# Performance work log

Hardware: AMD Instinct MI355X
Metric: run time of the kernel (lower is better)

The kernel has to match this reference:

```python
import jax, jax.numpy as jnp
import numpy as np

N_NODES = 156
NFEAT = 256
NHID = 128
B = 16384
T = 24
HLSTM = 32
ALPHA = 0.2


def setup_inputs() -> dict:
    key = jax.random.key(0)
    ks = jax.random.split(key, 16)
    f32 = jnp.float32
    inp = {
        "embedding": jax.random.normal(ks[0], (N_NODES, NFEAT), f32),
        "x": jax.random.normal(ks[1], (B, T, N_NODES), f32),
        "adj": jax.random.randint(ks[2], (N_NODES, N_NODES), 0, 2, jnp.int32),
        # GAT params (xavier-ish scale)
        "W_recent": jax.random.normal(ks[3], (NFEAT, NHID), f32) * 0.08,
        "a_recent": jax.random.normal(ks[4], (2 * NHID, 1), f32) * 0.1,
        "W_period": jax.random.normal(ks[5], (NFEAT, NHID), f32) * 0.08,
        "a_period": jax.random.normal(ks[6], (2 * NHID, 1), f32) * 0.1,
        # LSTM params, torch layout: weight_ih [4H, D], weight_hh [4H, H]
        "Wih_r": jax.random.normal(ks[7], (4 * HLSTM, N_NODES), f32) * 0.08,
        "Whh_r": jax.random.normal(ks[8], (4 * HLSTM, HLSTM), f32) * 0.08,
        "bih_r": jnp.zeros((4 * HLSTM,), f32),
        "bhh_r": jnp.zeros((4 * HLSTM,), f32),
        "Wih_p": jax.random.normal(ks[9], (4 * HLSTM, N_NODES), f32) * 0.08,
        "Whh_p": jax.random.normal(ks[10], (4 * HLSTM, HLSTM), f32) * 0.08,
        "bih_p": jnp.zeros((4 * HLSTM,), f32),
        "bhh_p": jnp.zeros((4 * HLSTM,), f32),
        "fc_W": jax.random.normal(ks[11], (N_NODES, 2 * HLSTM), f32) * 0.1,
        "fc_b": jnp.zeros((N_NODES,), f32),
    }
    return inp


def _gat_attention(embedding, W, a, adj):
    # h = embedding @ W : [N, F]
    h = embedding @ W
    F = h.shape[1]
    # e[i,j] = leakyrelu(h_i . a[:F] + h_j . a[F:])  (same math as the
    # repeat/cat construction, without materializing [N*N, 2F])
    s1 = h @ a[:F, 0]   # [N]
    s2 = h @ a[F:, 0]   # [N]
    e = jax.nn.leaky_relu(s1[:, None] + s2[None, :], ALPHA)
    e = jnp.where(adj > 0, e, jnp.float32(-9e15))
    return jax.nn.softmax(e, axis=1)  # [N, N]


def _lstm_last(x_seq, Wih, Whh, bih, bhh):
    # x_seq: [B, T, D]; returns last hidden state [B, H]
    H = Whh.shape[1]
    Bn = x_seq.shape[0]
    h0 = jnp.zeros((Bn, H), x_seq.dtype)
    c0 = jnp.zeros((Bn, H), x_seq.dtype)
    bias = bih + bhh

    def step(carry, xt):
        h, c = carry
        g = xt @ Wih.T + h @ Whh.T + bias
        i, f, gg, o = jnp.split(g, 4, axis=-1)  # torch gate order i,f,g,o
        c = jax.nn.sigmoid(f) * c + jax.nn.sigmoid(i) * jnp.tanh(gg)
        h = jax.nn.sigmoid(o) * jnp.tanh(c)
        return (h, c), None

    (h, c), _ = jax.lax.scan(step, (h0, c0), jnp.swapaxes(x_seq, 0, 1))
    return h


def reference(embedding, x, adj, W_recent, a_recent, W_period, a_period,
              Wih_r, Whh_r, bih_r, bhh_r, Wih_p, Whh_p, bih_p, bhh_p,
              fc_W, fc_b):
    recent = x[:, :4, :]   # [B, 4, N]
    period = x[:, 4:, :]   # [B, T-4, N]

    # attention depends only on embedding/adj -> identical across timesteps
    attn_r = _gat_attention(embedding, W_recent, a_recent, adj)  # [N, N]
    attn_p = _gat_attention(embedding, W_period, a_period, adj)

    # out[b,t,i] = sum_j attn[i,j] * x[b,t,j]
    xr = jnp.einsum('ij,btj->bti', attn_r, recent)
    xp = jnp.einsum('ij,btj->bti', attn_p, period)

    hr = _lstm_last(xr, Wih_r, Whh_r, bih_r, bhh_r)  # [B, 32]
    hp = _lstm_last(xp, Wih_p, Whh_p, bih_p, bhh_p)  # [B, 32]

    h = jnp.concatenate([hr, hp], axis=1)            # [B, 64]
    return h @ fc_W.T + fc_b                         # [B, 156]
```

## Files before the change

### kernel.cpp

```cpp
#include <hip/hip_runtime.h>
#include <hip/hip_bf16.h>
#include <math.h>

#define N_NODES 156
#define NFEAT 256
#define NHID 128
#define BATCH 16384
#define TT 24
#define HLSTM 32
#define G4 128
#define ALPHA 0.2f
#define NW 2
#define ROWS_B (NW*16)

typedef __attribute__((ext_vector_type(8))) short bf16x8;
typedef __attribute__((ext_vector_type(4))) float f32x4;

static __device__ __forceinline__ unsigned short f2bf(float f) {
    unsigned u = __float_as_uint(f);
    u += 0x7fffu + ((u >> 16) & 1u);
    return (unsigned short)(u >> 16);
}
static __device__ __forceinline__ bf16x8 cv8(float4 a, float4 b) {
    union { __hip_bfloat16 h[8]; bf16x8 v; } u;
    u.h[0] = __float2bfloat16(a.x); u.h[1] = __float2bfloat16(a.y);
    u.h[2] = __float2bfloat16(a.z); u.h[3] = __float2bfloat16(a.w);
    u.h[4] = __float2bfloat16(b.x); u.h[5] = __float2bfloat16(b.y);
    u.h[6] = __float2bfloat16(b.z); u.h[7] = __float2bfloat16(b.w);
    return u.v;
}
static __device__ __forceinline__ float sigm(float x) { return 1.f / (1.f + __expf(-x)); }
static __device__ __forceinline__ float tanh_(float x) { return 1.f - 2.f / (__expf(2.f * x) + 1.f); }

__global__ void k_gat_s(const float* __restrict__ emb,
                        const float* __restrict__ Wr, const float* __restrict__ ar,
                        const float* __restrict__ Wp, const float* __restrict__ ap,
                        float* __restrict__ s_buf ) {
    int i = blockIdx.x;
    int gat = blockIdx.y;
    const float* W = gat ? Wp : Wr;
    const float* a = gat ? ap : ar;
    int j = threadIdx.x;
    __shared__ float erow[NFEAT];
    __shared__ float red[128];
    for (int k = j; k < NFEAT; k += 128) erow[k] = emb[i*NFEAT + k];
    __syncthreads();
    float h = 0.f;
    for (int k = 0; k < NFEAT; ++k) h = fmaf(erow[k], W[k*NHID + j], h);
    float v1 = h * a[j];
    float v2 = h * a[NHID + j];
    red[j] = v1; __syncthreads();
    for (int s = 64; s > 0; s >>= 1) { if (j < s) red[j] += red[j+s]; __syncthreads(); }
    if (j == 0) s_buf[(gat*2+0)*N_NODES + i] = red[0];
    __syncthreads();
    red[j] = v2; __syncthreads();
    for (int s = 64; s > 0; s >>= 1) { if (j < s) red[j] += red[j+s]; __syncthreads(); }
    if (j == 0) s_buf[(gat*2+1)*N_NODES + i] = red[0];
}

__global__ void k_attn(const float* __restrict__ s_buf, const int* __restrict__ adj,
                       float* __restrict__ attn ) {
    int i = blockIdx.x, gat = blockIdx.y;
    int j = threadIdx.x;
    __shared__ float red[256];
    float s1 = s_buf[(gat*2+0)*N_NODES + i];
    bool act = (j < N_NODES);
    float e = -INFINITY;
    if (act) {
        float s2 = s_buf[(gat*2+1)*N_NODES + j];
        float z = s1 + s2;
        z = (z > 0.f) ? z : ALPHA * z;
        if (adj[i*N_NODES + j] <= 0) z = -9e15f;
        e = z;
    }
    red[j] = e; __syncthreads();
    for (int s = 128; s > 0; s >>= 1) { if (j < s) red[j] = fmaxf(red[j], red[j+s]); __syncthreads(); }
    float m = red[0]; __syncthreads();
    float val = act ? __expf(e - m) : 0.f;
    red[j] = val; __syncthreads();
    for (int s = 128; s > 0; s >>= 1) { if (j < s) red[j] += red[j+s]; __syncthreads(); }
    float inv = 1.f / red[0];
    if (act) attn[(gat*N_NODES + i)*N_NODES + j] = val * inv;
}

__global__ void k_prep(const float* __restrict__ attn,
                       const float* __restrict__ Wih_r, const float* __restrict__ Wih_p,
                       const float* __restrict__ Whh_r, const float* __restrict__ Whh_p,
                       const float* __restrict__ bih_r, const float* __restrict__ bhh_r,
                       const float* __restrict__ bih_p, const float* __restrict__ bhh_p,
                       unsigned short* __restrict__ Mbf ,
                       unsigned short* __restrict__ Whhbf ,
                       float* __restrict__ bias2 ) {
    int g = blockIdx.x, gat = blockIdx.y;
    const float* Wih = gat ? Wih_p : Wih_r;
    const float* A = attn + gat*N_NODES*N_NODES;
    int j = threadIdx.x;
    if (j < 160) {
        float acc = 0.f;
        if (j < N_NODES)
            for (int n = 0; n < N_NODES; ++n)
                acc = fmaf(Wih[g*N_NODES + n], A[n*N_NODES + j], acc);
        Mbf[(gat*G4 + g)*160 + j] = f2bf(acc);
    }
    if (j < HLSTM)
        Whhbf[(gat*G4 + g)*HLSTM + j] = f2bf((gat ? Whh_p : Whh_r)[g*HLSTM + j]);
    if (g == 0 && j < G4)
        bias2[gat*G4 + j] = gat ? (bih_p[j] + bhh_p[j]) : (bih_r[j] + bhh_r[j]);
}

#define XS_W (5*64*8)
#define XS_B (NW*XS_W)
__global__ void __launch_bounds__(NW*64, 1)
k_fused(const float* __restrict__ x,
        const unsigned short* __restrict__ Mbf,
        const unsigned short* __restrict__ Whhbf,
        const float* __restrict__ bias2,
        const float* __restrict__ fcW,
        const float* __restrict__ fcb,
        float* __restrict__ out) {
    __shared__ __align__(16) unsigned short xs[2*XS_B];
    __shared__ __align__(16) unsigned short hfrag[NW*512];
    __shared__ __align__(16) unsigned short hcatf[NW*1024];

    const int tid = threadIdx.x;
    const int w  = tid >> 6;
    const int l  = tid & 63;
    const int lm = l & 15;
    const int lg = l >> 4;
    const int b0 = blockIdx.x * ROWS_B;
    const size_t xrow = (size_t)(b0 + 16*w + lm) * (TT*N_NODES);

    bf16x8 bfr[8][5];
    bf16x8 wrec[8];
    float  bias_v[8];
    float  cst[8];

#define LOAD_FRAGS(Mb, Wb, bs) do {                                          \
    _Pragma("unroll")                                                        \
    for (int nt = 0; nt < 8; ++nt) {                                         \
        int n_ = nt*16 + lm;                                                 \
        _Pragma("unroll")                                                    \
        for (int kf = 0; kf < 5; ++kf)                                       \
            bfr[nt][kf] = *(const bf16x8*)((Mb) + n_*160 + kf*32 + lg*8);    \
        wrec[nt]   = *(const bf16x8*)((Wb) + n_*HLSTM + lg*8);               \
        bias_v[nt] = (bs)[n_];                                               \
    } } while (0)

    #pragma unroll
    for (int ds = 0; ds < 2; ++ds)
        #pragma unroll
        for (int i = 0; i < 4; ++i) {
            hfrag[w*512 + ((lm>>3) + 2*ds)*128 + (lg*4 + i)*8 + (lm&7)] = 0;
            cst[ds*4 + i] = 0.f;
        }
    LOAD_FRAGS(Mbf, Whhbf, bias2);

    float4 fA[10], fB[10];
    const float4 f4z = make_float4(0.f, 0.f, 0.f, 0.f);

#define ISSUE(F, TL) do {                                                    \
    const float* bp_ = x + xrow + (size_t)(TL)*N_NODES + lg*8;               \
    _Pragma("unroll")                                                        \
    for (int kf = 0; kf < 5; ++kf) {                                         \
        F[2*kf]   = *(const float4*)(bp_ + kf*32);                           \
        F[2*kf+1] = (kf == 4 && lg == 3) ? f4z                               \
                                         : *(const float4*)(bp_ + kf*32 + 4);\
    } } while (0)

#define CVTW(F, NB) do {                                                     \
    unsigned short* xw_ = xs + (NB)*XS_B + w*XS_W + l*8;                     \
    _Pragma("unroll")                                                        \
    for (int kf = 0; kf < 5; ++kf)                                           \
        *(bf16x8*)(xw_ + kf*512) = cv8(F[2*kf], F[2*kf+1]);                  \
    } while (0)

    ISSUE(fA, 0);
    ISSUE(fB, 1);
    CVTW(fA, 0);

#define STEP(T_, FC, FN) do {                                                \
    if ((T_) + 2 < TT) ISSUE(FN, (T_) + 2);                                  \
    if ((T_) + 1 < TT) CVTW(FC, ((T_) + 1) & 1);       \
    f32x4 acc[8];                                                            \
    _Pragma("unroll")                                                        \
    for (int nt = 0; nt < 8; ++nt)                                           \
        acc[nt] = (f32x4){bias_v[nt], bias_v[nt], bias_v[nt], bias_v[nt]};   \
    { const unsigned short* xr_ = xs + ((T_)&1)*XS_B + w*XS_W + l*8;         \
      _Pragma("unroll")                                                      \
      for (int kf = 0; kf < 5; ++kf) {                                       \
          bf16x8 af = *(const bf16x8*)(xr_ + kf*512);                        \
          _Pragma("unroll")                                                  \
          for (int nt = 0; nt < 8; ++nt)                                     \
              acc[nt] = __builtin_amdgcn_mfma_f32_16x16x32_bf16(af, bfr[nt][kf], acc[nt], 0, 0, 0); \
      }                                                                      \
      bf16x8 hf = *(const bf16x8*)(hfrag + w*512 + l*8);                     \
      _Pragma("unroll")                                                      \
      for (int nt = 0; nt < 8; ++nt)                                         \
          acc[nt] = __builtin_amdgcn_mfma_f32_16x16x32_bf16(hf, wrec[nt], acc[nt], 0, 0, 0); \
    }                                                                        \
    _Pragma("unroll")                                                        \
    for (int ds = 0; ds < 2; ++ds)                                           \
        _Pragma("unroll")                                                    \
        for (int i = 0; i < 4; ++i) {                                        \
            float si = sigm(acc[0 + ds][i]);                                 \
            float sf = sigm(acc[2 + ds][i]);                                 \
            float tg = tanh_(acc[4 + ds][i]);                                \
            float so = sigm(acc[6 + ds][i]);                                 \
            float c  = sf * cst[ds*4 + i] + si * tg;                         \
            float h  = so * tanh_(c);                                        \
            int cidx = ((lm>>3) + 2*ds)*128 + (lg*4 + i)*8 + (lm&7);         \
            if ((T_) == 3) {               \
                hcatf[w*1024 + cidx] = f2bf(h);                              \
                hfrag[w*512 + cidx]  = 0;                                    \
                cst[ds*4 + i] = 0.f;                                         \
            } else {                                                         \
                cst[ds*4 + i] = c;                                           \
                hfrag[w*512 + cidx] = f2bf(h);                               \
                if ((T_) == TT-1) hcatf[w*1024 + 512 + cidx] = f2bf(h);      \
            }                                                                \
        }                                                                    \
    if ((T_) == 3) LOAD_FRAGS(Mbf + G4*160, Whhbf + G4*HLSTM, bias2 + G4);   \
    } while (0)

    for (int t = 0; t < TT; t += 2) {
        STEP(t,     fB, fA);
        STEP(t + 1, fA, fB);
    }

    {
        bf16x8 ha0 = *(const bf16x8*)(hcatf + w*1024 + l*8);
        bf16x8 ha1 = *(const bf16x8*)(hcatf + w*1024 + 512 + l*8);
        #pragma unroll
        for (int nt = 0; nt < 10; ++nt) {
            int n  = nt*16 + lm;
            int nc = n < 155 ? n : 155;
            const float* wp0 = fcW + nc*64 + lg*8;
            const float* wp1 = fcW + nc*64 + 32 + lg*8;
            bf16x8 wf0 = cv8(*(const float4*)wp0, *(const float4*)(wp0 + 4));
            bf16x8 wf1 = cv8(*(const float4*)wp1, *(const float4*)(wp1 + 4));
            f32x4 fa = (f32x4){0.f, 0.f, 0.f, 0.f};
            fa = __builtin_amdgcn_mfma_f32_16x16x32_bf16(ha0, wf0, fa, 0, 0, 0);
            fa = __builtin_amdgcn_mfma_f32_16x16x32_bf16(ha1, wf1, fa, 0, 0, 0);
            if (n < N_NODES) {
                float bn = fcb[n];
                #pragma unroll
                for (int i = 0; i < 4; ++i)
                    out[(size_t)(b0 + 16*w + lg*4 + i)*N_NODES + n] = fa[i] + bn;
            }
        }
    }
#undef STEP
#undef CVTW
#undef ISSUE
#undef LOAD_FRAGS
}

extern "C" void kernel_launch(void* const* d_in, const int* in_sizes, int n_in,
                              void* d_out, int out_size, void* d_ws, size_t ws_size,
                              hipStream_t stream) {
    (void)in_sizes; (void)n_in; (void)out_size; (void)ws_size;
    const float* emb   = (const float*)d_in[0];
    const float* x     = (const float*)d_in[1];
    const int*   adj   = (const int*)d_in[2];
    const float* Wr    = (const float*)d_in[3];
    const float* ar    = (const float*)d_in[4];
    const float* Wp    = (const float*)d_in[5];
    const float* ap    = (const float*)d_in[6];
    const float* Wih_r = (const float*)d_in[7];
    const float* Whh_r = (const float*)d_in[8];
    const float* bih_r = (const float*)d_in[9];
    const float* bhh_r = (const float*)d_in[10];
    const float* Wih_p = (const float*)d_in[11];
    const float* Whh_p = (const float*)d_in[12];
    const float* bih_p = (const float*)d_in[13];
    const float* bhh_p = (const float*)d_in[14];
    const float* fcW   = (const float*)d_in[15];
    const float* fcb   = (const float*)d_in[16];
    float* out = (float*)d_out;

    char* ws = (char*)d_ws;
    size_t off = 0;
    auto alloc = [&](size_t bytes) {
        char* p = ws + off;
        off += (bytes + 255) & ~(size_t)255;
        return p;
    };
    float*          attn  = (float*)alloc(2*156*156*sizeof(float));
    float*          sbuf  = (float*)alloc(4*156*sizeof(float));
    unsigned short* Mbf   = (unsigned short*)alloc(2*G4*160*sizeof(unsigned short));
    unsigned short* Whhbf = (unsigned short*)alloc(2*G4*HLSTM*sizeof(unsigned short));
    float*          bias2 = (float*)alloc(2*G4*sizeof(float));

    k_gat_s<<<dim3(156, 2), 128, 0, stream>>>(emb, Wr, ar, Wp, ap, sbuf);
    k_attn<<<dim3(156, 2), 256, 0, stream>>>(sbuf, adj, attn);
    k_prep<<<dim3(128, 2), 192, 0, stream>>>(attn, Wih_r, Wih_p, Whh_r, Whh_p,
                                             bih_r, bhh_r, bih_p, bhh_p,
                                             Mbf, Whhbf, bias2);
    k_fused<<<dim3(BATCH/ROWS_B), NW*64, 0, stream>>>(x, Mbf, Whhbf, bias2, fcW, fcb, out);
}
```

Baseline: 97.62 us.

## Stream x timesteps into LDS via direct global_load_lds with triple buffering

Replaces the register-staged x loads (global to registers, convert to bf16, write to LDS) with direct global-to-LDS async loads of raw fp32 rows into a three-slot ring buffer per wave. Conversion to bf16 happens after reading from LDS, just before the MFMAs. Loads are issued three timesteps ahead, with explicit vmcnt waits. The goal is to cut register pressure and VALU/LDS-write work in the load path and deepen latency hiding. In exchange it uses more LDS, relies on hand-tuned waitcnt counts that are fragile if the compiler reorders, and reads unaligned row offsets from LDS.

Result: faster. 94.19 us (-3.5%).

```diff
diff --git a/kernel.cpp b/kernel.cpp
--- a/kernel.cpp
+++ b/kernel.cpp
@@ -12,6 +12,8 @@
 #define ALPHA 0.2f
 #define NW 2
 #define ROWS_B (NW*16)
+#define XSTRIDE (TT*N_NODES)
+#define SLOTF 2560
 
 typedef __attribute__((ext_vector_type(8))) short bf16x8;
 typedef __attribute__((ext_vector_type(4))) float f32x4;
@@ -108,8 +110,6 @@
         bias2[gat*G4 + j] = gat ? (bih_p[j] + bhh_p[j]) : (bih_r[j] + bhh_r[j]);
 }
 
-#define XS_W (5*64*8)
-#define XS_B (NW*XS_W)
 __global__ void __launch_bounds__(NW*64, 1)
 k_fused(const float* __restrict__ x,
         const unsigned short* __restrict__ Mbf,
@@ -118,7 +118,7 @@
         const float* __restrict__ fcW,
         const float* __restrict__ fcb,
         float* __restrict__ out) {
-    __shared__ __align__(16) unsigned short xs[2*XS_B];
+    __shared__ __align__(16) float xsf[NW][3][SLOTF];
     __shared__ __align__(16) unsigned short hfrag[NW*512];
     __shared__ __align__(16) unsigned short hcatf[NW*1024];
 
@@ -128,12 +128,23 @@
     const int lm = l & 15;
     const int lg = l >> 4;
     const int b0 = blockIdx.x * ROWS_B;
-    const size_t xrow = (size_t)(b0 + 16*w + lm) * (TT*N_NODES);
+
+    unsigned goff[10];
+    #pragma unroll
+    for (int i = 0; i < 10; ++i) {
+        int c = l + i*64;
+        int r = c / 39;
+        int cf = (c - r*39) * 4;
+        if (r > 15) r = 15;
+        goff[i] = (unsigned)(r*XSTRIDE + cf);
+    }
+    const float* xg = x + (size_t)(b0 + 16*w) * XSTRIDE;
 
     bf16x8 bfr[8][5];
     bf16x8 wrec[8];
     float  bias_v[8];
     float  cst[8];
+    const float4 f4z = make_float4(0.f, 0.f, 0.f, 0.f);
 
 #define LOAD_FRAGS(Mb, Wb, bs) do {                                          \
     _Pragma("unroll")                                                        \
@@ -155,77 +166,85 @@
         }
     LOAD_FRAGS(Mbf, Whhbf, bias2);
 
-    float4 fA[10], fB[10];
-    const float4 f4z = make_float4(0.f, 0.f, 0.f, 0.f);
-
-#define ISSUE(F, TL) do {                                                    \
-    const float* bp_ = x + xrow + (size_t)(TL)*N_NODES + lg*8;               \
-    _Pragma("unroll")                                                        \
-    for (int kf = 0; kf < 5; ++kf) {                                         \
-        F[2*kf]   = *(const float4*)(bp_ + kf*32);                           \
-        F[2*kf+1] = (kf == 4 && lg == 3) ? f4z                               \
-                                         : *(const float4*)(bp_ + kf*32 + 4);\
-    } } while (0)
-
-#define CVTW(F, NB) do {                                                     \
-    unsigned short* xw_ = xs + (NB)*XS_B + w*XS_W + l*8;                     \
-    _Pragma("unroll")                                                        \
-    for (int kf = 0; kf < 5; ++kf)                                           \
-        *(bf16x8*)(xw_ + kf*512) = cv8(F[2*kf], F[2*kf+1]);                  \
+#define DMA_STEP(S_, T_) do {                                                 \
+    const float* gp_ = xg + (T_)*N_NODES;                                     \
+    _Pragma("unroll")                                                         \
+    for (int i_ = 0; i_ < 10; ++i_)                                           \
+        __builtin_amdgcn_global_load_lds(                                     \
+            (const __attribute__((address_space(1))) void*)(gp_ + goff[i_]),  \
+            (__attribute__((address_space(3))) void*)(&xsf[w][S_][i_*256]),   \
+            16, 0, 0);                                                        \
     } while (0)
 
-    ISSUE(fA, 0);
-    ISSUE(fB, 1);
-    CVTW(fA, 0);
-
-#define STEP(T_, FC, FN) do {                                                \
-    if ((T_) + 2 < TT) ISSUE(FN, (T_) + 2);                                  \
-    if ((T_) + 1 < TT) CVTW(FC, ((T_) + 1) & 1);       \
-    f32x4 acc[8];                                                            \
-    _Pragma("unroll")                                                        \
-    for (int nt = 0; nt < 8; ++nt)                                           \
-        acc[nt] = (f32x4){bias_v[nt], bias_v[nt], bias_v[nt], bias_v[nt]};   \
-    { const unsigned short* xr_ = xs + ((T_)&1)*XS_B + w*XS_W + l*8;         \
-      _Pragma("unroll")                                                      \
-      for (int kf = 0; kf < 5; ++kf) {                                       \
-          bf16x8 af = *(const bf16x8*)(xr_ + kf*512);                        \
-          _Pragma("unroll")                                                  \
-          for (int nt = 0; nt < 8; ++nt)                                     \
-              acc[nt] = __builtin_amdgcn_mfma_f32_16x16x32_bf16(af, bfr[nt][kf], acc[nt], 0, 0, 0); \
-      }                                                                      \
-      bf16x8 hf = *(const bf16x8*)(hfrag + w*512 + l*8);                     \
-      _Pragma("unroll")                                                      \
-      for (int nt = 0; nt < 8; ++nt)                                         \
-          acc[nt] = __builtin_amdgcn_mfma_f32_16x16x32_bf16(hf, wrec[nt], acc[nt], 0, 0, 0); \
-    }                                                                        \
-    _Pragma("unroll")                                                        \
-    for (int ds = 0; ds < 2; ++ds)                                           \
-        _Pragma("unroll")                                                    \
-        for (int i = 0; i < 4; ++i) {                                        \
-            float si = sigm(acc[0 + ds][i]);                                 \
-            float sf = sigm(acc[2 + ds][i]);                                 \
-            float tg = tanh_(acc[4 + ds][i]);                                \
-            float so = sigm(acc[6 + ds][i]);                                 \
-            float c  = sf * cst[ds*4 + i] + si * tg;                         \
-            float h  = so * tanh_(c);                                        \
-            int cidx = ((lm>>3) + 2*ds)*128 + (lg*4 + i)*8 + (lm&7);         \
-            if ((T_) == 3) {               \
-                hcatf[w*1024 + cidx] = f2bf(h);                              \
-                hfrag[w*512 + cidx]  = 0;                                    \
-                cst[ds*4 + i] = 0.f;                                         \
-            } else {                                                         \
-                cst[ds*4 + i] = c;                                           \
-                hfrag[w*512 + cidx] = f2bf(h);                               \
-                if ((T_) == TT-1) hcatf[w*1024 + 512 + cidx] = f2bf(h);      \
-            }                                                                \
-        }                                                                    \
-    if ((T_) == 3) LOAD_FRAGS(Mbf + G4*160, Whhbf + G4*HLSTM, bias2 + G4);   \
+#define WAITVM(N_) asm volatile("s_waitcnt vmcnt(" #N_ ")" ::: "memory")
+
+#define STEP(S_, T_, ISS_, TN_) do {                                          \
+    const float* xr_ = &xsf[w][S_][0] + lm*N_NODES + lg*8;                    \
+    float4 q0_[5], q1_[5];                                                    \
+    _Pragma("unroll")                                                         \
+    for (int kf = 0; kf < 5; ++kf) {                                          \
+        q0_[kf] = *(const float4*)(xr_ + kf*32);                              \
+        q1_[kf] = *(const float4*)(xr_ + kf*32 + 4);                          \
+    }                                                                         \
+    bf16x8 hf_ = *(const bf16x8*)(hfrag + w*512 + l*8);                       \
+    if (lg == 3) q1_[4] = f4z;                       \
+    bf16x8 af_[5];                                                            \
+    _Pragma("unroll")                                                         \
+    for (int kf = 0; kf < 5; ++kf) af_[kf] = cv8(q0_[kf], q1_[kf]);           \
+    asm volatile("s_waitcnt lgkmcnt(0)" ::: "memory");                        \
+    __builtin_amdgcn_sched_barrier(0);                                        \
+    if (ISS_) DMA_STEP(S_, TN_);                \
+    f32x4 acc[8];                                                             \
+    _Pragma("unroll")                                                         \
+    for (int nt = 0; nt < 8; ++nt)                                            \
+        acc[nt] = (f32x4){bias_v[nt], bias_v[nt], bias_v[nt], bias_v[nt]};    \
+    _Pragma("unroll")                                                         \
+    for (int kf = 0; kf < 5; ++kf)                                            \
+        _Pragma("unroll")                                                     \
+        for (int nt = 0; nt < 8; ++nt)                                        \
+            acc[nt] = __builtin_amdgcn_mfma_f32_16x16x32_bf16(af_[kf], bfr[nt][kf], acc[nt], 0, 0, 0); \
+    _Pragma("unroll")                                                         \
+    for (int nt = 0; nt < 8; ++nt)                                            \
+        acc[nt] = __builtin_amdgcn_mfma_f32_16x16x32_bf16(hf_, wrec[nt], acc[nt], 0, 0, 0); \
+    _Pragma("unroll")                                                         \
+    for (int ds = 0; ds < 2; ++ds)                                            \
+        _Pragma("unroll")                                                     \
+        for (int i = 0; i < 4; ++i) {                                         \
+            float si = sigm(acc[0 + ds][i]);                                  \
+            float sf = sigm(acc[2 + ds][i]);                                  \
+            float tg = tanh_(acc[4 + ds][i]);                                 \
+            float so = sigm(acc[6 + ds][i]);                                  \
+            float c  = sf * cst[ds*4 + i] + si * tg;                          \
+            float h  = so * tanh_(c);                                         \
+            int cidx = ((lm>>3) + 2*ds)*128 + (lg*4 + i)*8 + (lm&7);          \
+            if ((T_) == 3) {                \
+                hcatf[w*1024 + cidx] = f2bf(h);                               \
+                hfrag[w*512 + cidx]  = 0;                                     \
+                cst[ds*4 + i] = 0.f;                                          \
+            } else {                                                          \
+                cst[ds*4 + i] = c;                                            \
+                hfrag[w*512 + cidx] = f2bf(h);                                \
+                if ((T_) == TT-1) hcatf[w*1024 + 512 + cidx] = f2bf(h);       \
+            }                                                                 \
+        }                                                                     \
+    if ((T_) == 3) LOAD_FRAGS(Mbf + G4*160, Whhbf + G4*HLSTM, bias2 + G4);    \
     } while (0)
 
-    for (int t = 0; t < TT; t += 2) {
-        STEP(t,     fB, fA);
-        STEP(t + 1, fA, fB);
-    }
+    DMA_STEP(0, 0);
+    DMA_STEP(1, 1);
+    DMA_STEP(2, 2);
+
+    int s = 0;
+    #pragma unroll 3
+    for (int t = 0; t < TT-2; ++t) {
+        WAITVM(20);
+        STEP(s, t, (t < TT-3), t+3);
+        s = (s == 2) ? 0 : s + 1;
+    }
+    WAITVM(10);
+    STEP(1, TT-2, 0, 0);
+    WAITVM(0);
+    STEP(2, TT-1, 0, 0);
 
     {
         bf16x8 ha0 = *(const bf16x8*)(hcatf + w*1024 + l*8);
@@ -250,8 +269,8 @@
         }
     }
 #undef STEP
-#undef CVTW
-#undef ISSUE
+#undef WAITVM
+#undef DMA_STEP
 #undef LOAD_FRAGS
 }
 
```

## Split fused LSTM into parallel input-projection GEMM and recurrent scan kernel

Applied to the files above, without the earlier changes.

Replaces the single fused kernel, which did the input projection and the recurrence step by step, with two kernels. The first is a batched MFMA GEMM over all timesteps that writes fp16 gate preactivations to a workspace buffer. The second is a lightweight scan kernel that streams those preactivations with prefetch and runs only the recurrent MFMA and the gate math. This takes the large input GEMM off the serial dependency chain and raises parallelism, at the cost of an extra round trip through global memory of about 100 MB of fp16 and reduced precision on the preactivations.

Result: slower. 185.0 us (+89.6%).

```diff
diff --git a/kernel.cpp b/kernel.cpp
--- a/kernel.cpp
+++ b/kernel.cpp
@@ -1,5 +1,6 @@
 #include <hip/hip_runtime.h>
 #include <hip/hip_bf16.h>
+#include <hip/hip_fp16.h>
 #include <math.h>
 
 #define N_NODES 156
@@ -10,8 +11,8 @@
 #define HLSTM 32
 #define G4 128
 #define ALPHA 0.2f
-#define NW 2
-#define ROWS_B (NW*16)
+#define XSTRIDE (TT*N_NODES)
+#define APAD 172
 
 typedef __attribute__((ext_vector_type(8))) short bf16x8;
 typedef __attribute__((ext_vector_type(4))) float f32x4;
@@ -108,128 +109,175 @@
         bias2[gat*G4 + j] = gat ? (bih_p[j] + bhh_p[j]) : (bih_r[j] + bhh_r[j]);
 }
 
-#define XS_W (5*64*8)
-#define XS_B (NW*XS_W)
-__global__ void __launch_bounds__(NW*64, 1)
-k_fused(const float* __restrict__ x,
-        const unsigned short* __restrict__ Mbf,
-        const unsigned short* __restrict__ Whhbf,
-        const float* __restrict__ bias2,
-        const float* __restrict__ fcW,
-        const float* __restrict__ fcb,
-        float* __restrict__ out) {
-    __shared__ __align__(16) unsigned short xs[2*XS_B];
-    __shared__ __align__(16) unsigned short hfrag[NW*512];
-    __shared__ __align__(16) unsigned short hcatf[NW*1024];
+__global__ void __launch_bounds__(256, 2)
+k_gemm(const float* __restrict__ x,
+       const unsigned short* __restrict__ Mbf,
+       unsigned short* __restrict__ gbuf) {
+    __shared__ __align__(16) unsigned short As[128*APAD];
 
     const int tid = threadIdx.x;
     const int w  = tid >> 6;
     const int l  = tid & 63;
     const int lm = l & 15;
     const int lg = l >> 4;
-    const int b0 = blockIdx.x * ROWS_B;
-    const size_t xrow = (size_t)(b0 + 16*w + lm) * (TT*N_NODES);
-
-    bf16x8 bfr[8][5];
+    const int mhalf = w >> 1, nhalf = w & 1;
+    const int bg = blockIdx.x, tg = blockIdx.y;
+
+    const float* xbase = x + (size_t)bg*16*XSTRIDE + tg*1248;
+    #pragma unroll 4
+    for (int idx = tid; idx < 4992; idx += 256) {
+        int row = idx / 312, rem = idx - row*312;
+        float4 v = *(const float4*)(xbase + (size_t)row*XSTRIDE + rem*4);
+        int trel = rem / 39, c4 = rem - trel*39;
+        union { __hip_bfloat16 h[4]; uint2 u; } cv;
+        cv.h[0] = __float2bfloat16(v.x); cv.h[1] = __float2bfloat16(v.y);
+        cv.h[2] = __float2bfloat16(v.z); cv.h[3] = __float2bfloat16(v.w);
+        *(uint2*)(As + (trel*16 + row)*APAD + c4*4) = cv.u;
+    }
+    if (tid < 128) *(uint2*)(As + tid*APAD + 156) = make_uint2(0u, 0u);
+    __syncthreads();
+
+    const unsigned short* Mb = Mbf + ((tg == 0 && mhalf == 0) ? 0 : G4*160);
+    bf16x8 bfr[4][5];
+    #pragma unroll
+    for (int ni = 0; ni < 4; ++ni) {
+        int n_ = (nhalf*4 + ni)*16 + lm;
+        #pragma unroll
+        for (int kf = 0; kf < 5; ++kf)
+            bfr[ni][kf] = *(const bf16x8*)(Mb + n_*160 + kf*32 + lg*8);
+    }
+
+    f32x4 acc[4][4];
+    #pragma unroll
+    for (int mi = 0; mi < 4; ++mi)
+        #pragma unroll
+        for (int ni = 0; ni < 4; ++ni) acc[mi][ni] = (f32x4){0.f, 0.f, 0.f, 0.f};
+
+    #pragma unroll
+    for (int kf = 0; kf < 5; ++kf) {
+        bf16x8 af[4];
+        #pragma unroll
+        for (int mi = 0; mi < 4; ++mi)
+            af[mi] = *(const bf16x8*)(As + ((mhalf*4 + mi)*16 + lm)*APAD + kf*32 + lg*8);
+        #pragma unroll
+        for (int mi = 0; mi < 4; ++mi)
+            #pragma unroll
+            for (int ni = 0; ni < 4; ++ni)
+                acc[mi][ni] = __builtin_amdgcn_mfma_f32_16x16x32_bf16(af[mi], bfr[ni][kf], acc[mi][ni], 0, 0, 0);
+    }
+
+    #pragma unroll
+    for (int mi = 0; mi < 4; ++mi) {
+        int t = tg*8 + mhalf*4 + mi;
+        #pragma unroll
+        for (int ni = 0; ni < 4; ++ni) {
+            int nt = nhalf*4 + ni;
+            union { __half h[4]; uint2 u; } p;
+            p.h[0] = __float2half(acc[mi][ni][0]);
+            p.h[1] = __float2half(acc[mi][ni][1]);
+            p.h[2] = __float2half(acc[mi][ni][2]);
+            p.h[3] = __float2half(acc[mi][ni][3]);
+            *(uint2*)((char*)gbuf + ((((size_t)bg*24 + t)*8 + nt) << 9) + l*8) = p.u;
+        }
+    }
+}
+
+__global__ void __launch_bounds__(64, 1)
+k_scan(const unsigned short* __restrict__ gbuf,
+       const unsigned short* __restrict__ Whhbf,
+       const float* __restrict__ bias2,
+       const float* __restrict__ fcW,
+       const float* __restrict__ fcb,
+       float* __restrict__ out) {
+    __shared__ __align__(16) unsigned short hfr[512];
+    __shared__ __align__(16) unsigned short hcat[16*72];
+
+    const int l  = threadIdx.x;
+    const int lm = l & 15;
+    const int lg = l >> 4;
+    const int bg = blockIdx.x;
+    const int b0 = bg * 16;
+    const char* gb = (const char*)gbuf;
+
     bf16x8 wrec[8];
     float  bias_v[8];
     float  cst[8];
-
-#define LOAD_FRAGS(Mb, Wb, bs) do {                                          \
+    unsigned short hrv[8], hpv[8];
+
+#define LOAD_WB(Wb, bs) do {                                                 \
     _Pragma("unroll")                                                        \
     for (int nt = 0; nt < 8; ++nt) {                                         \
         int n_ = nt*16 + lm;                                                 \
-        _Pragma("unroll")                                                    \
-        for (int kf = 0; kf < 5; ++kf)                                       \
-            bfr[nt][kf] = *(const bf16x8*)((Mb) + n_*160 + kf*32 + lg*8);    \
         wrec[nt]   = *(const bf16x8*)((Wb) + n_*HLSTM + lg*8);               \
         bias_v[nt] = (bs)[n_];                                               \
     } } while (0)
 
-    #pragma unroll
-    for (int ds = 0; ds < 2; ++ds)
-        #pragma unroll
-        for (int i = 0; i < 4; ++i) {
-            hfrag[w*512 + ((lm>>3) + 2*ds)*128 + (lg*4 + i)*8 + (lm&7)] = 0;
-            cst[ds*4 + i] = 0.f;
-        }
-    LOAD_FRAGS(Mbf, Whhbf, bias2);
-
-    float4 fA[10], fB[10];
-    const float4 f4z = make_float4(0.f, 0.f, 0.f, 0.f);
-
-#define ISSUE(F, TL) do {                                                    \
-    const float* bp_ = x + xrow + (size_t)(TL)*N_NODES + lg*8;               \
-    _Pragma("unroll")                                                        \
-    for (int kf = 0; kf < 5; ++kf) {                                         \
-        F[2*kf]   = *(const float4*)(bp_ + kf*32);                           \
-        F[2*kf+1] = (kf == 4 && lg == 3) ? f4z                               \
-                                         : *(const float4*)(bp_ + kf*32 + 4);\
-    } } while (0)
-
-#define CVTW(F, NB) do {                                                     \
-    unsigned short* xw_ = xs + (NB)*XS_B + w*XS_W + l*8;                     \
-    _Pragma("unroll")                                                        \
-    for (int kf = 0; kf < 5; ++kf)                                           \
-        *(bf16x8*)(xw_ + kf*512) = cv8(F[2*kf], F[2*kf+1]);                  \
+#define LOADG(R_, T_) do {                                                   \
+    _Pragma("unroll")                                                        \
+    for (int nt = 0; nt < 8; ++nt)                                           \
+        R_[nt] = *(const uint2*)(gb + ((((size_t)bg*24 + (T_))*8 + nt) << 9) + l*8); \
     } while (0)
 
-    ISSUE(fA, 0);
-    ISSUE(fB, 1);
-    CVTW(fA, 0);
-
-#define STEP(T_, FC, FN) do {                                                \
-    if ((T_) + 2 < TT) ISSUE(FN, (T_) + 2);                                  \
-    if ((T_) + 1 < TT) CVTW(FC, ((T_) + 1) & 1);       \
+#define STEP(T_, GC_) do {                                                   \
+    bf16x8 hf_ = *(const bf16x8*)(hfr + l*8);                                \
     f32x4 acc[8];                                                            \
     _Pragma("unroll")                                                        \
+    for (int nt = 0; nt < 8; ++nt) {                                         \
+        const __half2* hp_ = (const __half2*)&GC_[nt];                       \
+        float2 f01 = __half22float2(hp_[0]);                                 \
+        float2 f23 = __half22float2(hp_[1]);                                 \
+        acc[nt] = (f32x4){bias_v[nt] + f01.x, bias_v[nt] + f01.y,            \
+                          bias_v[nt] + f23.x, bias_v[nt] + f23.y};           \
+    }                                                                        \
+    _Pragma("unroll")                                                        \
     for (int nt = 0; nt < 8; ++nt)                                           \
-        acc[nt] = (f32x4){bias_v[nt], bias_v[nt], bias_v[nt], bias_v[nt]};   \
-    { const unsigned short* xr_ = xs + ((T_)&1)*XS_B + w*XS_W + l*8;         \
-      _Pragma("unroll")                                                      \
-      for (int kf = 0; kf < 5; ++kf) {                                       \
-          bf16x8 af = *(const bf16x8*)(xr_ + kf*512);                        \
-          _Pragma("unroll")                                                  \
-          for (int nt = 0; nt < 8; ++nt)                                     \
-              acc[nt] = __builtin_amdgcn_mfma_f32_16x16x32_bf16(af, bfr[nt][kf], acc[nt], 0, 0, 0); \
-      }                                                                      \
-      bf16x8 hf = *(const bf16x8*)(hfrag + w*512 + l*8);                     \
-      _Pragma("unroll")                                                      \
-      for (int nt = 0; nt < 8; ++nt)                                         \
-          acc[nt] = __builtin_amdgcn_mfma_f32_16x16x32_bf16(hf, wrec[nt], acc[nt], 0, 0, 0); \
-    }                                                                        \
+        acc[nt] = __builtin_amdgcn_mfma_f32_16x16x32_bf16(hf_, wrec[nt], acc[nt], 0, 0, 0); \
     _Pragma("unroll")                                                        \
     for (int ds = 0; ds < 2; ++ds)                                           \
         _Pragma("unroll")                                                    \
         for (int i = 0; i < 4; ++i) {                                        \
+            int v = ds*4 + i;                                                \
             float si = sigm(acc[0 + ds][i]);                                 \
             float sf = sigm(acc[2 + ds][i]);                                 \
             float tg = tanh_(acc[4 + ds][i]);                                \
             float so = sigm(acc[6 + ds][i]);                                 \
-            float c  = sf * cst[ds*4 + i] + si * tg;                         \
-            float h  = so * tanh_(c);                                        \
+            float c  = sf*cst[v] + si*tg;                                    \
+            float h  = so*tanh_(c);                                          \
             int cidx = ((lm>>3) + 2*ds)*128 + (lg*4 + i)*8 + (lm&7);         \
-            if ((T_) == 3) {               \
-                hcatf[w*1024 + cidx] = f2bf(h);                              \
-                hfrag[w*512 + cidx]  = 0;                                    \
-                cst[ds*4 + i] = 0.f;                                         \
-            } else {                                                         \
-                cst[ds*4 + i] = c;                                           \
-                hfrag[w*512 + cidx] = f2bf(h);                               \
-                if ((T_) == TT-1) hcatf[w*1024 + 512 + cidx] = f2bf(h);      \
-            }                                                                \
+            if ((T_) == 3)           { hrv[v] = f2bf(h); hfr[cidx] = 0; cst[v] = 0.f; } \
+            else if ((T_) == TT-1)   { hpv[v] = f2bf(h); }                   \
+            else                     { cst[v] = c; hfr[cidx] = f2bf(h); }    \
         }                                                                    \
-    if ((T_) == 3) LOAD_FRAGS(Mbf + G4*160, Whhbf + G4*HLSTM, bias2 + G4);   \
+    if ((T_) == 3) LOAD_WB(Whhbf + G4*HLSTM, bias2 + G4);                    \
     } while (0)
 
+    LOAD_WB(Whhbf, bias2);
+    #pragma unroll
+    for (int v = 0; v < 8; ++v) cst[v] = 0.f;
+    #pragma unroll
+    for (int j = 0; j < 8; ++j) hfr[l*8 + j] = 0;
+
+    uint2 gA[8], gB[8];
+    LOADG(gA, 0);
     for (int t = 0; t < TT; t += 2) {
-        STEP(t,     fB, fA);
-        STEP(t + 1, fA, fB);
-    }
-
+        if (t + 1 < TT) LOADG(gB, t + 1);
+        STEP(t, gA);
+        if (t + 2 < TT) LOADG(gA, t + 2);
+        if (t + 1 < TT) STEP(t + 1, gB);
+    }
+
+    #pragma unroll
+    for (int ds = 0; ds < 2; ++ds)
+        #pragma unroll
+        for (int i = 0; i < 4; ++i) {
+            int r = lg*4 + i, d = lm + 16*ds, v = ds*4 + i;
+            hcat[r*72 + d]      = hrv[v];
+            hcat[r*72 + 32 + d] = hpv[v];
+        }
+    __builtin_amdgcn_s_barrier();
     {
-        bf16x8 ha0 = *(const bf16x8*)(hcatf + w*1024 + l*8);
-        bf16x8 ha1 = *(const bf16x8*)(hcatf + w*1024 + 512 + l*8);
+        bf16x8 ha0 = *(const bf16x8*)(hcat + lm*72 + lg*8);
+        bf16x8 ha1 = *(const bf16x8*)(hcat + lm*72 + 32 + lg*8);
         #pragma unroll
         for (int nt = 0; nt < 10; ++nt) {
             int n  = nt*16 + lm;
@@ -245,14 +293,13 @@
                 float bn = fcb[n];
                 #pragma unroll
                 for (int i = 0; i < 4; ++i)
-                    out[(size_t)(b0 + 16*w + lg*4 + i)*N_NODES + n] = fa[i] + bn;
+                    out[(size_t)(b0 + lg*4 + i)*N_NODES + n] = fa[i] + bn;
             }
         }
     }
 #undef STEP
-#undef CVTW
-#undef ISSUE
-#undef LOAD_FRAGS
+#undef LOADG
+#undef LOAD_WB
 }
 
 extern "C" void kernel_launch(void* const* d_in, const int* in_sizes, int n_in,
@@ -290,11 +337,13 @@
     unsigned short* Mbf   = (unsigned short*)alloc(2*G4*160*sizeof(unsigned short));
     unsigned short* Whhbf = (unsigned short*)alloc(2*G4*HLSTM*sizeof(unsigned short));
     float*          bias2 = (float*)alloc(2*G4*sizeof(float));
+    unsigned short* gbuf  = (unsigned short*)alloc((size_t)BATCH*TT*G4*2);
 
     k_gat_s<<<dim3(156, 2), 128, 0, stream>>>(emb, Wr, ar, Wp, ap, sbuf);
     k_attn<<<dim3(156, 2), 256, 0, stream>>>(sbuf, adj, attn);
     k_prep<<<dim3(128, 2), 192, 0, stream>>>(attn, Wih_r, Wih_p, Whh_r, Whh_p,
                                              bih_r, bhh_r, bih_p, bhh_p,
                                              Mbf, Whhbf, bias2);
-    k_fused<<<dim3(BATCH/ROWS_B), NW*64, 0, stream>>>(x, Mbf, Whhbf, bias2, fcW, fcb, out);
-}
+    k_gemm<<<dim3(BATCH/16, TT/8), 256, 0, stream>>>(x, Mbf, gbuf);
+    k_scan<<<dim3(BATCH/16), 64, 0, stream>>>(gbuf, Whhbf, bias2, fcW, fcb, out);
+}
```
